# Kernel optimization log

Measured on AMD Instinct MI355X. Metric: run time of the kernel, lower is better.

Reference implementation:

```python
import jax, jax.numpy as jnp
import numpy as np

B, S, D = 4, 4096, 1024          # batch, seq, in/out features
H = 128                          # controller_hidden_dim
K = 8                            # num_spectral_bases
R = 8                            # low_rank_rank
OR = 8                           # orthogonal_rank
RES_SCALE = 1.0; SPEC_SCALE = 1.0; LR_SCALE = 1.0; ROT_SCALE = 1.0
LN_EPS = 1e-5


def setup_inputs() -> dict:
    key = jax.random.key(0)
    ks = jax.random.split(key, 16)
    g = lambda k, shape, scale=0.02: jax.random.normal(k, shape, jnp.float32) * scale
    return dict(
        x=jax.random.normal(ks[0], (B, S, D), jnp.float32),
        # base linear (teacher-aligned base)
        W_base=g(ks[1], (D, D)), b_base=jnp.zeros((D,), jnp.float32),
        # pooled-token conditioner: LayerNorm -> Linear -> GELU -> Linear
        ln_g=jnp.ones((D,), jnp.float32), ln_b=jnp.zeros((D,), jnp.float32),
        Wc1=g(ks[2], (D, H)), bc1=jnp.zeros((H,), jnp.float32),
        Wc2=g(ks[3], (H, H)), bc2=jnp.zeros((H,), jnp.float32),
        # gate heads
        W_rot_gate=g(ks[4], (H, 1)), b_rot_gate=jnp.zeros((1,), jnp.float32),
        W_rot_coeff=g(ks[5], (H, OR)), b_rot_coeff=jnp.zeros((OR,), jnp.float32),
        W_spec_gate=g(ks[6], (H, K)), b_spec_gate=jnp.zeros((K,), jnp.float32),
        W_lr_coeff=g(ks[7], (H, R)), b_lr_coeff=jnp.zeros((R,), jnp.float32),
        # spectral basis operator: input basis U, output basis V
        U_spec=g(ks[8], (K, D), 0.05), V_spec=g(ks[9], (K, D), 0.05),
        # low-rank residual operator
        U_lr=g(ks[10], (R, D), 0.05), V_lr=g(ks[11], (R, D), 0.05),
        # low-rank orthogonal mixer generators (skew-symmetric pairs)
        A_orth=g(ks[12], (OR, D), 0.05), B_orth=g(ks[13], (OR, D), 0.05),
    )


def reference(x, W_base, b_base, ln_g, ln_b, Wc1, bc1, Wc2, bc2,
              W_rot_gate, b_rot_gate, W_rot_coeff, b_rot_coeff,
              W_spec_gate, b_spec_gate, W_lr_coeff, b_lr_coeff,
              U_spec, V_spec, U_lr, V_lr, A_orth, B_orth):
    # --- pooled token conditioner: mean pool -> LN -> MLP -> hidden h [B,H]
    pooled = x.mean(axis=1)                                   # [B, D]
    mu = pooled.mean(-1, keepdims=True)
    var = pooled.var(-1, keepdims=True)
    z = (pooled - mu) * jax.lax.rsqrt(var + LN_EPS) * ln_g + ln_b
    h = jax.nn.gelu(z @ Wc1 + bc1) @ Wc2 + bc2                # [B, H]

    # --- conditioner-produced gates
    rot_gate = jax.nn.sigmoid(h @ W_rot_gate + b_rot_gate)    # [B, 1]
    rot_coeff = jnp.tanh(h @ W_rot_coeff + b_rot_coeff)       # [B, OR]
    spec_gate = jnp.tanh(h @ W_spec_gate + b_spec_gate)       # [B, K]
    lr_coeff = jnp.tanh(h @ W_lr_coeff + b_lr_coeff)          # [B, R]

    # --- low-rank orthogonal mixer: x_rot = x + gate * x @ G^T,
    #     G = sum_k c_k (a_k b_k^T - b_k a_k^T) (skew-symmetric generator)
    pa = jnp.einsum('bsi,ki->bsk', x, A_orth)
    pb = jnp.einsum('bsi,ki->bsk', x, B_orth)
    rot = (jnp.einsum('bsk,bk,ki->bsi', pb, rot_coeff, A_orth)
           - jnp.einsum('bsk,bk,ki->bsi', pa, rot_coeff, B_orth))
    x_rot = x + (ROT_SCALE * rot_gate)[:, None, :] * rot      # [B,S,D]

    # --- spectral basis operator: gated rank-K map through fixed bases
    s = jnp.einsum('bsi,ki->bsk', x_rot, U_spec)
    y_spec = SPEC_SCALE * jnp.einsum('bsk,bk,ko->bso', s, spec_gate, V_spec)

    # --- low-rank residual operator
    t = jnp.einsum('bsi,ki->bsk', x_rot, U_lr)
    y_lr = LR_SCALE * jnp.einsum('bsk,bk,ko->bso', t, lr_coeff, V_lr)

    # --- teacher-aligned base + gated residual operators
    return x_rot @ W_base + b_base + RES_SCALE * (y_spec + y_lr)
```

## Files before the change

kernel.cpp:

```cpp
#include <hip/hip_runtime.h>

typedef unsigned short u16;
typedef unsigned int   u32;
typedef __bf16 bf16x8 __attribute__((ext_vector_type(8)));
typedef float  f32x4  __attribute__((ext_vector_type(4)));

#define DD 1024

__device__ __forceinline__ u16 f2bf(float f) {
  u32 u = __float_as_uint(f);
  u32 r = (u + 0x7FFFu + ((u >> 16) & 1u)) >> 16;
  return (u16)r;
}

typedef const __attribute__((address_space(1))) void* gp1;
typedef __attribute__((address_space(3))) void* lp3;
__device__ __forceinline__ void gll16(const void* g, void* l) {
  __builtin_amdgcn_global_load_lds((gp1)g, (lp3)l, 16, 0, 0);
}

template <bool XB>
__global__ __launch_bounds__(256) void k01_pre(
    const float* __restrict__ x, u16* __restrict__ xb, float* __restrict__ pooled,
    const float* __restrict__ W,
    const float* __restrict__ Ao, const float* __restrict__ Bo,
    const float* __restrict__ Us, const float* __restrict__ Ul,
    float* __restrict__ AWBW, float* __restrict__ Mbuf,
    u16* __restrict__ Pb, u16* __restrict__ Wt) {
  const int tid = threadIdx.x;
  int bid = blockIdx.x;
  if (bid < 256) {
    const int b = bid >> 6;
    const long r0 = (long)bid * 64;
    const int c0 = tid * 4;
    float s0 = 0.f, s1 = 0.f, s2 = 0.f, s3 = 0.f;
    for (int r = 0; r < 64; r++) {
      float4 v = *(const float4*)(x + (r0 + r) * DD + c0);
      if (XB) {
        ushort4 o;
        o.x = f2bf(v.x); o.y = f2bf(v.y); o.z = f2bf(v.z); o.w = f2bf(v.w);
        *(ushort4*)(xb + (r0 + r) * DD + c0) = o;
      }
      s0 += v.x; s1 += v.y; s2 += v.z; s3 += v.w;
    }
    atomicAdd(&pooled[b * DD + c0 + 0], s0);
    atomicAdd(&pooled[b * DD + c0 + 1], s1);
    atomicAdd(&pooled[b * DD + c0 + 2], s2);
    atomicAdd(&pooled[b * DD + c0 + 3], s3);
    return;
  }
  bid -= 256;
  if (bid < 32) {
    __shared__ float red2[2][128][16];
    const int m = bid;
    const int n = (m & 7) * 128 + (tid & 127), q = m >> 3, ih = tid >> 7;
    float acc[16];
#pragma unroll
    for (int k = 0; k < 16; k++) acc[k] = 0.f;
    const int ib = q * 256 + ih * 128;
    for (int i = ib; i < ib + 128; i++) {
      float wv = W[(long)i * DD + n];
#pragma unroll
      for (int k = 0; k < 8; k++) {
        acc[k]     += Ao[k * DD + i] * wv;
        acc[k + 8] += Bo[k * DD + i] * wv;
      }
    }
#pragma unroll
    for (int k = 0; k < 16; k++) red2[ih][tid & 127][k] = acc[k];
    __syncthreads();
    if (ih == 0)
#pragma unroll
      for (int k = 0; k < 16; k++)
        atomicAdd(&AWBW[k * DD + n], red2[0][tid][k] + red2[1][tid][k]);
  } else if (bid < 36) {
    __shared__ float red[64][4];
    const int m = bid - 32;
    const float* L  = (m == 0 || m == 2) ? Ao : Bo;
    const float* Rr = (m < 2) ? Us : Ul;
    const int o = tid >> 2, ch = tid & 3;
    const int k = o >> 3, kp = o & 7;
    float a = 0.f;
    for (int i = ch * 256; i < ch * 256 + 256; i++)
      a += L[(long)k * DD + i] * Rr[(long)kp * DD + i];
    red[o][ch] = a;
    __syncthreads();
    if (tid < 64) Mbuf[m * 64 + tid] = red[tid][0] + red[tid][1] + red[tid][2] + red[tid][3];
  } else if (bid < 40) {
    const int m = bid - 36;
    const float* src = m == 0 ? Ao : m == 1 ? Bo : m == 2 ? Us : Ul;
#pragma unroll
    for (int j = 0; j < 8; j++)
      for (int q = 0; q < 4; q++) {
        int i = q * 256 + tid;
        Pb[(m * 8 + j) * DD + i] = f2bf(src[j * DD + i]);
      }
  } else {
    __shared__ u16 T[64][66];
    const int t = bid - 40, tr = t >> 4, tc = t & 15;
#pragma unroll
    for (int q2 = 0; q2 < 16; q2++) {
      int idx = q2 * 256 + tid, r = idx >> 6, c = idx & 63;
      T[r][c] = f2bf(W[(long)(tr * 64 + r) * DD + tc * 64 + c]);
    }
    __syncthreads();
#pragma unroll
    for (int q2 = 0; q2 < 16; q2++) {
      int idx = q2 * 256 + tid, c = idx >> 6, r = idx & 63;
      Wt[(long)(tc * 64 + c) * DD + tr * 64 + r] = T[r][c];
    }
  }
}

__global__ __launch_bounds__(256) void k2a_h1(
    const float* __restrict__ pooledsum,
    const float* __restrict__ lng, const float* __restrict__ lnb,
    const float* __restrict__ Wc1, float* __restrict__ h1pre) {
  __shared__ float zs[1024];
  __shared__ float wsh[16384];
  __shared__ float red[256];
  const int tid = threadIdx.x;
  const int b = blockIdx.x >> 3, ch = blockIdx.x & 7;
  float4 v = *(const float4*)(pooledsum + b * DD + tid * 4);
  v.x *= (1.f / 4096.f); v.y *= (1.f / 4096.f); v.z *= (1.f / 4096.f); v.w *= (1.f / 4096.f);
  float s = v.x + v.y + v.z + v.w;
  float sq = v.x * v.x + v.y * v.y + v.z * v.z + v.w * v.w;
  red[tid] = s; __syncthreads();
  for (int st = 128; st > 0; st >>= 1) { if (tid < st) red[tid] += red[tid + st]; __syncthreads(); }
  float mu = red[0] * (1.f / 1024.f);
  __syncthreads();
  red[tid] = sq; __syncthreads();
  for (int st = 128; st > 0; st >>= 1) { if (tid < st) red[tid] += red[tid + st]; __syncthreads(); }
  float var = red[0] * (1.f / 1024.f) - mu * mu;
  float rs = rsqrtf(var + 1e-5f);
  __syncthreads();
  {
    float4 g = *(const float4*)(lng + tid * 4);
    float4 be = *(const float4*)(lnb + tid * 4);
    zs[tid * 4 + 0] = (v.x - mu) * rs * g.x + be.x;
    zs[tid * 4 + 1] = (v.y - mu) * rs * g.y + be.y;
    zs[tid * 4 + 2] = (v.z - mu) * rs * g.z + be.z;
    zs[tid * 4 + 3] = (v.w - mu) * rs * g.w + be.w;
  }
  {
    const float4* src = (const float4*)(Wc1 + ch * 16384);
    float4* dst = (float4*)wsh;
#pragma unroll
    for (int it = 0; it < 16; it++) dst[it * 256 + tid] = src[it * 256 + tid];
  }
  __syncthreads();
  const int j = tid & 127, half = tid >> 7;
  float a = 0.f;
#pragma unroll 8
  for (int dd = 0; dd < 64; dd++) {
    int ldi = half * 64 + dd;
    a += zs[ch * 128 + ldi] * wsh[ldi * 128 + j];
  }
  red[tid] = a;
  __syncthreads();
  if (tid < 128) atomicAdd(&h1pre[b * 128 + tid], red[tid] + red[tid + 128]);
}

__global__ __launch_bounds__(256) void k2b_gates_pack(
    const float* __restrict__ h1pre, const float* __restrict__ AWBW,
    const float* Vs, const float* Vl,
    const float* bc1, const float* Wc2, const float* bc2,
    const float* Wrg, const float* brg, const float* Wrc, const float* brc,
    const float* Wsg, const float* bsg, const float* Wlc, const float* blc,
    float* __restrict__ gates, u16* __restrict__ RwT) {
  const int tid = threadIdx.x;
  if (blockIdx.x < 4) {
    __shared__ float wc2sh[16384];
    __shared__ float h1s[128], hb[128];
    __shared__ float red[256];
    __shared__ float hw[3200];
    const int b = blockIdx.x;
    {
      const float4* src = (const float4*)Wc2;
      float4* dst = (float4*)wc2sh;
#pragma unroll
      for (int it = 0; it < 16; it++) dst[it * 256 + tid] = src[it * 256 + tid];
    }
    for (int idx = tid; idx < 3200; idx += 256) {
      float vv;
      if (idx < 128)       vv = Wrg[idx];
      else if (idx < 1152) vv = Wrc[idx - 128];
      else if (idx < 2176) vv = Wsg[idx - 1152];
      else                 vv = Wlc[idx - 2176];
      hw[idx] = vv;
    }
    if (tid < 128) {
      float hv = h1pre[b * 128 + tid] + bc1[tid];
      float th = tanhf(0.7978845608028654f * (hv + 0.044715f * hv * hv * hv));
      h1s[tid] = 0.5f * hv * (1.f + th);
    }
    __syncthreads();
    const int i = tid & 127, half = tid >> 7;
    float a = 0.f;
#pragma unroll 8
    for (int k = 0; k < 64; k++) {
      int kk = half * 64 + k;
      a += h1s[kk] * wc2sh[kk * 128 + i];
    }
    red[tid] = a;
    __syncthreads();
    if (tid < 128) hb[tid] = red[tid] + red[tid + 128] + bc2[tid];
    __syncthreads();
    if (tid < 25) {
      float acc;
      if (tid == 0) {
        acc = brg[0];
        for (int k = 0; k < 128; k++) acc += hb[k] * hw[k];
        red[0] = 1.f / (1.f + expf(-acc));
      } else if (tid < 9) {
        int ci = tid - 1; acc = brc[ci];
        for (int k = 0; k < 128; k++) acc += hb[k] * hw[128 + k * 8 + ci];
        red[tid] = tanhf(acc);
      } else if (tid < 17) {
        int ci = tid - 9; acc = bsg[ci];
        for (int k = 0; k < 128; k++) acc += hb[k] * hw[1152 + k * 8 + ci];
        red[tid] = tanhf(acc);
      } else {
        int ci = tid - 17; acc = blc[ci];
        for (int k = 0; k < 128; k++) acc += hb[k] * hw[2176 + k * 8 + ci];
        red[tid] = tanhf(acc);
      }
    }
    __syncthreads();
    if (tid < 24) {
      float g = red[0];
      gates[b * 32 + tid] = (tid < 8) ? g * red[1 + tid] : red[1 + tid];
    }
  } else {
    const int n = (int)(blockIdx.x - 4) * 256 + tid;
#pragma unroll
    for (int j = 0; j < 8; j++) {
      RwT[n * 32 + j]      = f2bf(AWBW[j * DD + n]);
      RwT[n * 32 + 8 + j]  = f2bf(AWBW[(8 + j) * DD + n]);
      RwT[n * 32 + 16 + j] = f2bf(Vs[(long)j * DD + n]);
      RwT[n * 32 + 24 + j] = f2bf(Vl[(long)j * DD + n]);
    }
  }
}

__global__ __launch_bounds__(256, 3) void k3a_fused(
    const u16* __restrict__ xb, const u16* __restrict__ Wt,
    const u16* __restrict__ Pb, const float* __restrict__ gates,
    const float* __restrict__ Mbuf, const u16* __restrict__ RwT,
    const float* __restrict__ bb, float* __restrict__ out) {
  __shared__ __align__(16) char smem[38912];
  const int tid = threadIdx.x, lane = tid & 63, w = tid >> 6;
  const int quad = lane >> 4, lrow = lane & 15;
  const int bn = blockIdx.x & 7, bm = blockIdx.x >> 3;
  const long m0 = (long)bm * 128;
  const int n0 = bn * 128;
  const int batch = bm >> 5;
  float* Ml = (float*)(smem + 36864);
  float* gl = (float*)(smem + 37888);
  Ml[tid] = Mbuf[tid];
  if (tid < 24) gl[tid] = gates[batch * 32 + tid];
  const int mw = (w & 1) * 64, nw = (w >> 1) * 64;
  const int sr = lane >> 2, sc = (lane & 3) * 16;
  const char* xbp = (const char*)xb;
  const char* wtp = (const char*)Wt;
  const char* pbp = (const char*)Pb;
  const long aOff0 = (m0 + (long)w * 16 + sr) * 2048 + sc;
  const long aOff1 = aOff0 + 4 * 16 * 2048;
  const long bOff0 = ((long)n0 + w * 16 + sr) * 2048 + sc;
  const long bOff1 = bOff0 + 4 * 16 * 2048;
  const long pOff  = ((long)w * 16 + sr) * 2048 + sc;
  const int d0 = w * 1024 + lane * 16;

  f32x4 acc[4][4] = {};
  f32x4 acc2[2][2] = {};

  gll16(xbp + aOff0, smem + d0);
  gll16(xbp + aOff1, smem + d0 + 4096);
  gll16(wtp + bOff0, smem + 16384 + d0);
  gll16(wtp + bOff1, smem + 16384 + d0 + 4096);
  if (w < 2) gll16(pbp + pOff, smem + 32768 + d0);
  __syncthreads();

  int cur = 0;
  for (int kc = 0; kc < 32; kc++) {
    if (kc < 31) {
      const long ko = (long)(kc + 1) * 64;
      const int s = cur ^ 1;
      gll16(xbp + aOff0 + ko, smem + s * 8192 + d0);
      gll16(xbp + aOff1 + ko, smem + s * 8192 + d0 + 4096);
      gll16(wtp + bOff0 + ko, smem + 16384 + s * 8192 + d0);
      gll16(wtp + bOff1 + ko, smem + 16384 + s * 8192 + d0 + 4096);
      if (w < 2) gll16(pbp + pOff + ko, smem + 32768 + s * 2048 + d0);
    }
    const u16* At = (const u16*)(smem + cur * 8192);
    const u16* Bt = (const u16*)(smem + 16384 + cur * 8192);
    const u16* Pt = (const u16*)(smem + 32768 + cur * 2048);
    bf16x8 af[4], bq[4], af2[2], bp[2];
#pragma unroll
    for (int tm = 0; tm < 4; tm++)
      af[tm] = *(const bf16x8*)(At + (mw + tm * 16 + lrow) * 32 + quad * 8);
#pragma unroll
    for (int tn = 0; tn < 4; tn++)
      bq[tn] = *(const bf16x8*)(Bt + (nw + tn * 16 + lrow) * 32 + quad * 8);
#pragma unroll
    for (int t2 = 0; t2 < 2; t2++)
      af2[t2] = *(const bf16x8*)(At + (w * 32 + t2 * 16 + lrow) * 32 + quad * 8);
#pragma unroll
    for (int tn2 = 0; tn2 < 2; tn2++)
      bp[tn2] = *(const bf16x8*)(Pt + (tn2 * 16 + lrow) * 32 + quad * 8);
#pragma unroll
    for (int tm = 0; tm < 4; tm++)
#pragma unroll
      for (int tn = 0; tn < 4; tn++)
        acc[tm][tn] = __builtin_amdgcn_mfma_f32_16x16x32_bf16(af[tm], bq[tn], acc[tm][tn], 0, 0, 0);
#pragma unroll
    for (int t2 = 0; t2 < 2; t2++)
#pragma unroll
      for (int tn2 = 0; tn2 < 2; tn2++)
        acc2[t2][tn2] = __builtin_amdgcn_mfma_f32_16x16x32_bf16(af2[t2], bp[tn2], acc2[t2][tn2], 0, 0, 0);
    __syncthreads();
    cur ^= 1;
  }

  {
    const char* rwp = (const char*)RwT;
    const long rOff = ((long)n0 + w * 16 + sr) * 64 + sc;
    gll16(rwp + rOff, smem + 16384 + d0);
    gll16(rwp + rOff + 64 * 64, smem + 16384 + d0 + 4096);
  }
  float* projF = (float*)smem;
#pragma unroll
  for (int t2 = 0; t2 < 2; t2++)
#pragma unroll
    for (int tn2 = 0; tn2 < 2; tn2++)
#pragma unroll
      for (int r = 0; r < 4; r++)
        projF[(w * 32 + t2 * 16 + quad * 4 + r) * 32 + tn2 * 16 + lrow] = acc2[t2][tn2][r];
  __syncthreads();
  if (tid < 128) {
    float pr[32];
#pragma unroll
    for (int j = 0; j < 32; j++) pr[j] = projF[tid * 32 + j];
    float wo[32];
#pragma unroll
    for (int k = 0; k < 8; k++) { wo[k] = gl[k] * pr[8 + k]; wo[8 + k] = -gl[k] * pr[k]; }
#pragma unroll
    for (int kp = 0; kp < 8; kp++) {
      float sv = pr[16 + kp], tv = pr[24 + kp];
#pragma unroll
      for (int k = 0; k < 8; k++) {
        float gpb = gl[k] * pr[8 + k], gpa = gl[k] * pr[k];
        sv += gpb * Ml[k * 8 + kp]       - gpa * Ml[64 + k * 8 + kp];
        tv += gpb * Ml[128 + k * 8 + kp] - gpa * Ml[192 + k * 8 + kp];
      }
      wo[16 + kp] = gl[8 + kp] * sv;
      wo[24 + kp] = gl[16 + kp] * tv;
    }
    u16* wLds = (u16*)(smem + 24576);
#pragma unroll
    for (int j = 0; j < 32; j++) wLds[tid * 32 + j] = f2bf(wo[j]);
  }
  __syncthreads();
  {
    const u16* wL = (const u16*)(smem + 24576);
    const u16* Rt = (const u16*)(smem + 16384);
    bf16x8 af[4], bq[4];
#pragma unroll
    for (int tm = 0; tm < 4; tm++)
      af[tm] = *(const bf16x8*)(wL + (mw + tm * 16 + lrow) * 32 + quad * 8);
#pragma unroll
    for (int tn = 0; tn < 4; tn++)
      bq[tn] = *(const bf16x8*)(Rt + (nw + tn * 16 + lrow) * 32 + quad * 8);
#pragma unroll
    for (int tm = 0; tm < 4; tm++)
#pragma unroll
      for (int tn = 0; tn < 4; tn++)
        acc[tm][tn] = __builtin_amdgcn_mfma_f32_16x16x32_bf16(af[tm], bq[tn], acc[tm][tn], 0, 0, 0);
  }
#pragma unroll
  for (int tn = 0; tn < 4; tn++) {
    const int col = n0 + nw + tn * 16 + lrow;
    const float bias = bb[col];
#pragma unroll
    for (int tm = 0; tm < 4; tm++)
#pragma unroll
      for (int r = 0; r < 4; r++) {
        long row = m0 + mw + tm * 16 + quad * 4 + r;
        out[row * DD + col] = acc[tm][tn][r] + bias;
      }
  }
}

template <bool XB>
__global__ __launch_bounds__(256) void k3_fused(
    const float* __restrict__ xf, const u16* __restrict__ xb,
    const u16* __restrict__ Wt, const u16* __restrict__ Pb,
    const float* __restrict__ gates, const float* __restrict__ Mbuf,
    const u16* __restrict__ RwT, const float* __restrict__ bb,
    float* __restrict__ out) {
  __shared__ __align__(16) u16 At[4096];
  __shared__ __align__(16) u16 Bt[4096];
  __shared__ __align__(16) u16 Pt[1024];
  __shared__ float projF[128 * 32];
  __shared__ __align__(16) u16 wLds[4096];
  __shared__ float Ml[256];
  __shared__ float gl[24];
  const int tid = threadIdx.x, lane = tid & 63, w = tid >> 6;
  const int quad = lane >> 4, lrow = lane & 15;
  const int bn = blockIdx.x & 7, bm = blockIdx.x >> 3;
  const long m0 = (long)bm * 128;
  const int n0 = bn * 128;
  const int batch = bm >> 5;
  Ml[tid] = Mbuf[tid];
  if (tid < 24) gl[tid] = gates[batch * 32 + tid];
  const int mw = (w & 1) * 64, nw = (w >> 1) * 64;
  const int p0 = (w * 2) * 1024 + lane * 16, p1 = p0 + 1024;
  f32x4 acc[4][4] = {};
  f32x4 acc2[2][2] = {};
  for (int kc = 0; kc < 32; kc++) {
    uint4 vb0 = *(const uint4*)((const char*)Wt + (long)(n0 + (p0 >> 6)) * 2048 + kc * 64 + (p0 & 63));
    uint4 vb1 = *(const uint4*)((const char*)Wt + (long)(n0 + (p1 >> 6)) * 2048 + kc * 64 + (p1 & 63));
    uint4 vp;
    if (tid < 128)
      vp = *(const uint4*)((const char*)Pb + (tid >> 2) * 2048 + kc * 64 + (tid & 3) * 16);
    if (XB) {
      uint4 va0 = *(const uint4*)((const char*)xb + (m0 + (p0 >> 6)) * 2048 + kc * 64 + (p0 & 63));
      uint4 va1 = *(const uint4*)((const char*)xb + (m0 + (p1 >> 6)) * 2048 + kc * 64 + (p1 & 63));
      *(uint4*)((char*)At + p0) = va0;
      *(uint4*)((char*)At + p1) = va1;
    } else {
      ushort4 oa[4];
#pragma unroll
      for (int i = 0; i < 4; i++) {
        int fi = i * 256 + tid, row = fi >> 3, c4 = (fi & 7) * 4;
        float4 v = *(const float4*)(xf + (m0 + row) * DD + kc * 32 + c4);
        oa[i].x = f2bf(v.x); oa[i].y = f2bf(v.y); oa[i].z = f2bf(v.z); oa[i].w = f2bf(v.w);
      }
#pragma unroll
      for (int i = 0; i < 4; i++) {
        int fi = i * 256 + tid, row = fi >> 3, c4 = (fi & 7) * 4;
        *(ushort4*)(At + row * 32 + c4) = oa[i];
      }
    }
    *(uint4*)((char*)Bt + p0) = vb0;
    *(uint4*)((char*)Bt + p1) = vb1;
    if (tid < 128) *(uint4*)((char*)Pt + (tid >> 2) * 64 + (tid & 3) * 16) = vp;
    __syncthreads();
    bf16x8 af[4], bq[4], af2[2], bp[2];
#pragma unroll
    for (int tm = 0; tm < 4; tm++)
      af[tm] = *(const bf16x8*)(At + (mw + tm * 16 + lrow) * 32 + quad * 8);
#pragma unroll
    for (int tn = 0; tn < 4; tn++)
      bq[tn] = *(const bf16x8*)(Bt + (nw + tn * 16 + lrow) * 32 + quad * 8);
#pragma unroll
    for (int t2 = 0; t2 < 2; t2++)
      af2[t2] = *(const bf16x8*)(At + (w * 32 + t2 * 16 + lrow) * 32 + quad * 8);
#pragma unroll
    for (int tn2 = 0; tn2 < 2; tn2++)
      bp[tn2] = *(const bf16x8*)(Pt + (tn2 * 16 + lrow) * 32 + quad * 8);
#pragma unroll
    for (int tm = 0; tm < 4; tm++)
#pragma unroll
      for (int tn = 0; tn < 4; tn++)
        acc[tm][tn] = __builtin_amdgcn_mfma_f32_16x16x32_bf16(af[tm], bq[tn], acc[tm][tn], 0, 0, 0);
#pragma unroll
    for (int t2 = 0; t2 < 2; t2++)
#pragma unroll
      for (int tn2 = 0; tn2 < 2; tn2++)
        acc2[t2][tn2] = __builtin_amdgcn_mfma_f32_16x16x32_bf16(af2[t2], bp[tn2], acc2[t2][tn2], 0, 0, 0);
    __syncthreads();
  }
#pragma unroll
  for (int t2 = 0; t2 < 2; t2++)
#pragma unroll
    for (int tn2 = 0; tn2 < 2; tn2++)
#pragma unroll
      for (int r = 0; r < 4; r++)
        projF[(w * 32 + t2 * 16 + quad * 4 + r) * 32 + tn2 * 16 + lrow] = acc2[t2][tn2][r];
  {
    uint4 vr0 = *(const uint4*)((const char*)RwT + (long)(n0 + (p0 >> 6)) * 64 + (p0 & 63));
    uint4 vr1 = *(const uint4*)((const char*)RwT + (long)(n0 + (p1 >> 6)) * 64 + (p1 & 63));
    *(uint4*)((char*)Bt + p0) = vr0;
    *(uint4*)((char*)Bt + p1) = vr1;
  }
  __syncthreads();
  if (tid < 128) {
    float pr[32];
#pragma unroll
    for (int j = 0; j < 32; j++) pr[j] = projF[tid * 32 + j];
    float wo[32];
#pragma unroll
    for (int k = 0; k < 8; k++) { wo[k] = gl[k] * pr[8 + k]; wo[8 + k] = -gl[k] * pr[k]; }
#pragma unroll
    for (int kp = 0; kp < 8; kp++) {
      float sv = pr[16 + kp], tv = pr[24 + kp];
#pragma unroll
      for (int k = 0; k < 8; k++) {
        float gpb = gl[k] * pr[8 + k], gpa = gl[k] * pr[k];
        sv += gpb * Ml[k * 8 + kp]       - gpa * Ml[64 + k * 8 + kp];
        tv += gpb * Ml[128 + k * 8 + kp] - gpa * Ml[192 + k * 8 + kp];
      }
      wo[16 + kp] = gl[8 + kp] * sv;
      wo[24 + kp] = gl[16 + kp] * tv;
    }
#pragma unroll
    for (int j = 0; j < 32; j++) wLds[tid * 32 + j] = f2bf(wo[j]);
  }
  __syncthreads();
  {
    bf16x8 af[4], bq[4];
#pragma unroll
    for (int tm = 0; tm < 4; tm++)
      af[tm] = *(const bf16x8*)(wLds + (mw + tm * 16 + lrow) * 32 + quad * 8);
#pragma unroll
    for (int tn = 0; tn < 4; tn++)
      bq[tn] = *(const bf16x8*)(Bt + (nw + tn * 16 + lrow) * 32 + quad * 8);
#pragma unroll
    for (int tm = 0; tm < 4; tm++)
#pragma unroll
      for (int tn = 0; tn < 4; tn++)
        acc[tm][tn] = __builtin_amdgcn_mfma_f32_16x16x32_bf16(af[tm], bq[tn], acc[tm][tn], 0, 0, 0);
  }
#pragma unroll
  for (int tn = 0; tn < 4; tn++) {
    const int col = n0 + nw + tn * 16 + lrow;
    const float bias = bb[col];
#pragma unroll
    for (int tm = 0; tm < 4; tm++)
#pragma unroll
      for (int r = 0; r < 4; r++) {
        long row = m0 + mw + tm * 16 + quad * 4 + r;
        out[row * DD + col] = acc[tm][tn][r] + bias;
      }
  }
}

extern "C" void kernel_launch(void* const* d_in, const int* in_sizes, int n_in,
                              void* d_out, int out_size, void* d_ws, size_t ws_size,
                              hipStream_t stream) {
  const float* x   = (const float*)d_in[0];
  const float* Wb  = (const float*)d_in[1];
  const float* bb  = (const float*)d_in[2];
  const float* lng = (const float*)d_in[3];
  const float* lnb = (const float*)d_in[4];
  const float* Wc1 = (const float*)d_in[5];
  const float* bc1 = (const float*)d_in[6];
  const float* Wc2 = (const float*)d_in[7];
  const float* bc2 = (const float*)d_in[8];
  const float* Wrg = (const float*)d_in[9];
  const float* brg = (const float*)d_in[10];
  const float* Wrc = (const float*)d_in[11];
  const float* brc = (const float*)d_in[12];
  const float* Wsg = (const float*)d_in[13];
  const float* bsg = (const float*)d_in[14];
  const float* Wlc = (const float*)d_in[15];
  const float* blc = (const float*)d_in[16];
  const float* Us  = (const float*)d_in[17];
  const float* Vs  = (const float*)d_in[18];
  const float* Ul  = (const float*)d_in[19];
  const float* Vl  = (const float*)d_in[20];
  const float* Ao  = (const float*)d_in[21];
  const float* Bo  = (const float*)d_in[22];

  char* ws = (char*)d_ws;
  float* pooled = (float*)(ws + 0);
  float* AWBW   = (float*)(ws + 16384);
  float* h1pre  = (float*)(ws + 81920);
  float* gates  = (float*)(ws + 83968);
  float* Mbuf   = (float*)(ws + 84480);
  u16*   RwT    = (u16*)  (ws + 85504);
  u16*   Pb     = (u16*)  (ws + 151040);
  u16*   Wt     = (u16*)  (ws + 216576);
  u16*   xb     = (u16*)  (ws + 2313728);
  float* out    = (float*)d_out;

  const bool modeA = ws_size >= (size_t)2313728 + 33554432;

  (void)hipMemsetAsync(d_ws, 0, 83968, stream);
  if (modeA)
    k01_pre<true><<<552, 256, 0, stream>>>(x, xb, pooled, Wb, Ao, Bo, Us, Ul,
                                           AWBW, Mbuf, Pb, Wt);
  else
    k01_pre<false><<<552, 256, 0, stream>>>(x, xb, pooled, Wb, Ao, Bo, Us, Ul,
                                            AWBW, Mbuf, Pb, Wt);
  k2a_h1<<<32, 256, 0, stream>>>(pooled, lng, lnb, Wc1, h1pre);
  k2b_gates_pack<<<8, 256, 0, stream>>>(h1pre, AWBW, Vs, Vl,
                                        bc1, Wc2, bc2, Wrg, brg, Wrc, brc,
                                        Wsg, bsg, Wlc, blc, gates, RwT);
  if (modeA)
    k3a_fused<<<1024, 256, 0, stream>>>(xb, Wt, Pb, gates, Mbuf, RwT, bb, out);
  else
    k3_fused<false><<<1024, 256, 0, stream>>>(x, xb, Wt, Pb, gates, Mbuf, RwT, bb, out);
}
```

Baseline: 310.6 us.

## Fuse conditioner kernels via atomic counter and remap GEMM block order

Merges the h1 projection kernel and the gates/pack kernel into one launch. The gate blocks spin on a global atomic counter until all 32 h1 blocks have accumulated their partial sums, which removes one kernel launch and its inter-kernel gap. The fused GEMM kernel also remaps block indices so that consecutive blocks walk different M tiles while sharing N tiles, aiming for better L2 reuse of weights. The spin-wait assumes all 40 blocks are co-resident, which holds for 40 blocks on this GPU but is formally unsafe.

Measured after the change: 298.7 us. 3.9% less time.

```diff
diff --git a/kernel.cpp b/kernel.cpp
--- a/kernel.cpp
+++ b/kernel.cpp
@@ -112,69 +112,68 @@
   }
 }
 
-__global__ __launch_bounds__(256) void k2a_h1(
+__global__ __launch_bounds__(256) void k2ab(
     const float* __restrict__ pooledsum,
     const float* __restrict__ lng, const float* __restrict__ lnb,
-    const float* __restrict__ Wc1, float* __restrict__ h1pre) {
-  __shared__ float zs[1024];
-  __shared__ float wsh[16384];
-  __shared__ float red[256];
-  const int tid = threadIdx.x;
-  const int b = blockIdx.x >> 3, ch = blockIdx.x & 7;
-  float4 v = *(const float4*)(pooledsum + b * DD + tid * 4);
-  v.x *= (1.f / 4096.f); v.y *= (1.f / 4096.f); v.z *= (1.f / 4096.f); v.w *= (1.f / 4096.f);
-  float s = v.x + v.y + v.z + v.w;
-  float sq = v.x * v.x + v.y * v.y + v.z * v.z + v.w * v.w;
-  red[tid] = s; __syncthreads();
-  for (int st = 128; st > 0; st >>= 1) { if (tid < st) red[tid] += red[tid + st]; __syncthreads(); }
-  float mu = red[0] * (1.f / 1024.f);
-  __syncthreads();
-  red[tid] = sq; __syncthreads();
-  for (int st = 128; st > 0; st >>= 1) { if (tid < st) red[tid] += red[tid + st]; __syncthreads(); }
-  float var = red[0] * (1.f / 1024.f) - mu * mu;
-  float rs = rsqrtf(var + 1e-5f);
-  __syncthreads();
-  {
-    float4 g = *(const float4*)(lng + tid * 4);
-    float4 be = *(const float4*)(lnb + tid * 4);
-    zs[tid * 4 + 0] = (v.x - mu) * rs * g.x + be.x;
-    zs[tid * 4 + 1] = (v.y - mu) * rs * g.y + be.y;
-    zs[tid * 4 + 2] = (v.z - mu) * rs * g.z + be.z;
-    zs[tid * 4 + 3] = (v.w - mu) * rs * g.w + be.w;
-  }
-  {
-    const float4* src = (const float4*)(Wc1 + ch * 16384);
-    float4* dst = (float4*)wsh;
-#pragma unroll
-    for (int it = 0; it < 16; it++) dst[it * 256 + tid] = src[it * 256 + tid];
-  }
-  __syncthreads();
-  const int j = tid & 127, half = tid >> 7;
-  float a = 0.f;
-#pragma unroll 8
-  for (int dd = 0; dd < 64; dd++) {
-    int ldi = half * 64 + dd;
-    a += zs[ch * 128 + ldi] * wsh[ldi * 128 + j];
-  }
-  red[tid] = a;
-  __syncthreads();
-  if (tid < 128) atomicAdd(&h1pre[b * 128 + tid], red[tid] + red[tid + 128]);
-}
-
-__global__ __launch_bounds__(256) void k2b_gates_pack(
-    const float* __restrict__ h1pre, const float* __restrict__ AWBW,
-    const float* Vs, const float* Vl,
+    const float* __restrict__ Wc1, float* __restrict__ h1pre,
+    const float* __restrict__ AWBW, const float* Vs, const float* Vl,
     const float* bc1, const float* Wc2, const float* bc2,
     const float* Wrg, const float* brg, const float* Wrc, const float* brc,
     const float* Wsg, const float* bsg, const float* Wlc, const float* blc,
-    float* __restrict__ gates, u16* __restrict__ RwT) {
+    float* __restrict__ gates, u16* __restrict__ RwT,
+    u32* __restrict__ cnt) {
   const int tid = threadIdx.x;
-  if (blockIdx.x < 4) {
+  if (blockIdx.x < 32) {
+    __shared__ float zs[1024];
+    __shared__ float wsh[16384];
+    __shared__ float red[256];
+    const int b = blockIdx.x >> 3, ch = blockIdx.x & 7;
+    float4 v = *(const float4*)(pooledsum + b * DD + tid * 4);
+    v.x *= (1.f / 4096.f); v.y *= (1.f / 4096.f); v.z *= (1.f / 4096.f); v.w *= (1.f / 4096.f);
+    float s = v.x + v.y + v.z + v.w;
+    float sq = v.x * v.x + v.y * v.y + v.z * v.z + v.w * v.w;
+    red[tid] = s; __syncthreads();
+    for (int st = 128; st > 0; st >>= 1) { if (tid < st) red[tid] += red[tid + st]; __syncthreads(); }
+    float mu = red[0] * (1.f / 1024.f);
+    __syncthreads();
+    red[tid] = sq; __syncthreads();
+    for (int st = 128; st > 0; st >>= 1) { if (tid < st) red[tid] += red[tid + st]; __syncthreads(); }
+    float var = red[0] * (1.f / 1024.f) - mu * mu;
+    float rs = rsqrtf(var + 1e-5f);
+    __syncthreads();
+    {
+      float4 g = *(const float4*)(lng + tid * 4);
+      float4 be = *(const float4*)(lnb + tid * 4);
+      zs[tid * 4 + 0] = (v.x - mu) * rs * g.x + be.x;
+      zs[tid * 4 + 1] = (v.y - mu) * rs * g.y + be.y;
+      zs[tid * 4 + 2] = (v.z - mu) * rs * g.z + be.z;
+      zs[tid * 4 + 3] = (v.w - mu) * rs * g.w + be.w;
+    }
+    {
+      const float4* src = (const float4*)(Wc1 + ch * 16384);
+      float4* dst = (float4*)wsh;
+#pragma unroll
+      for (int it = 0; it < 16; it++) dst[it * 256 + tid] = src[it * 256 + tid];
+    }
+    __syncthreads();
+    const int j = tid & 127, half = tid >> 7;
+    float a = 0.f;
+#pragma unroll 8
+    for (int dd = 0; dd < 64; dd++) {
+      int ldi = half * 64 + dd;
+      a += zs[ch * 128 + ldi] * wsh[ldi * 128 + j];
+    }
+    red[tid] = a;
+    __syncthreads();
+    if (tid < 128) atomicAdd(&h1pre[b * 128 + tid], red[tid] + red[tid + 128]);
+    __syncthreads();
+    if (tid == 0) atomicAdd(cnt, 1u);
+  } else if (blockIdx.x < 36) {
     __shared__ float wc2sh[16384];
     __shared__ float h1s[128], hb[128];
     __shared__ float red[256];
     __shared__ float hw[3200];
-    const int b = blockIdx.x;
+    const int b = (int)blockIdx.x - 32;
     {
       const float4* src = (const float4*)Wc2;
       float4* dst = (float4*)wc2sh;
@@ -189,8 +188,12 @@
       else                 vv = Wlc[idx - 2176];
       hw[idx] = vv;
     }
+    if (tid == 0) {
+      while (atomicAdd(cnt, 0u) < 32u) __builtin_amdgcn_s_sleep(8);
+    }
+    __syncthreads();
     if (tid < 128) {
-      float hv = h1pre[b * 128 + tid] + bc1[tid];
+      float hv = atomicAdd(&h1pre[b * 128 + tid], 0.f) + bc1[tid];
       float th = tanhf(0.7978845608028654f * (hv + 0.044715f * hv * hv * hv));
       h1s[tid] = 0.5f * hv * (1.f + th);
     }
@@ -232,7 +235,7 @@
       gates[b * 32 + tid] = (tid < 8) ? g * red[1 + tid] : red[1 + tid];
     }
   } else {
-    const int n = (int)(blockIdx.x - 4) * 256 + tid;
+    const int n = (int)(blockIdx.x - 36) * 256 + tid;
 #pragma unroll
     for (int j = 0; j < 8; j++) {
       RwT[n * 32 + j]      = f2bf(AWBW[j * DD + n]);
@@ -251,7 +254,9 @@
   __shared__ __align__(16) char smem[38912];
   const int tid = threadIdx.x, lane = tid & 63, w = tid >> 6;
   const int quad = lane >> 4, lrow = lane & 15;
-  const int bn = blockIdx.x & 7, bm = blockIdx.x >> 3;
+  const int bidx = blockIdx.x;
+  const int bm = (bidx & 7) * 16 + (bidx >> 6);
+  const int bn = (bidx >> 3) & 7;
   const long m0 = (long)bm * 128;
   const int n0 = bn * 128;
   const int batch = bm >> 5;
@@ -569,25 +574,26 @@
   float* h1pre  = (float*)(ws + 81920);
   float* gates  = (float*)(ws + 83968);
   float* Mbuf   = (float*)(ws + 84480);
-  u16*   RwT    = (u16*)  (ws + 85504);
-  u16*   Pb     = (u16*)  (ws + 151040);
-  u16*   Wt     = (u16*)  (ws + 216576);
-  u16*   xb     = (u16*)  (ws + 2313728);
+  u32*   cnt    = (u32*)  (ws + 85504);
+  u16*   RwT    = (u16*)  (ws + 85568);
+  u16*   Pb     = (u16*)  (ws + 151104);
+  u16*   Wt     = (u16*)  (ws + 216640);
+  u16*   xb     = (u16*)  (ws + 2313792);
   float* out    = (float*)d_out;
 
-  const bool modeA = ws_size >= (size_t)2313728 + 33554432;
-
-  (void)hipMemsetAsync(d_ws, 0, 83968, stream);
+  const bool modeA = ws_size >= (size_t)2313792 + 33554432;
+
+  (void)hipMemsetAsync(d_ws, 0, 85568, stream);
   if (modeA)
     k01_pre<true><<<552, 256, 0, stream>>>(x, xb, pooled, Wb, Ao, Bo, Us, Ul,
                                            AWBW, Mbuf, Pb, Wt);
   else
     k01_pre<false><<<552, 256, 0, stream>>>(x, xb, pooled, Wb, Ao, Bo, Us, Ul,
                                             AWBW, Mbuf, Pb, Wt);
-  k2a_h1<<<32, 256, 0, stream>>>(pooled, lng, lnb, Wc1, h1pre);
-  k2b_gates_pack<<<8, 256, 0, stream>>>(h1pre, AWBW, Vs, Vl,
-                                        bc1, Wc2, bc2, Wrg, brg, Wrc, brc,
-                                        Wsg, bsg, Wlc, blc, gates, RwT);
+  k2ab<<<40, 256, 0, stream>>>(pooled, lng, lnb, Wc1, h1pre,
+                               AWBW, Vs, Vl, bc1, Wc2, bc2,
+                               Wrg, brg, Wrc, brc, Wsg, bsg, Wlc, blc,
+                               gates, RwT, cnt);
   if (modeA)
     k3a_fused<<<1024, 256, 0, stream>>>(xb, Wt, Pb, gates, Mbuf, RwT, bb, out);
   else
```
